# Kernel optimization log

Hardware: AMD Instinct MI355X
Metric: run time of the kernel (lower is better)

Reference implementation:

```python
import jax, jax.numpy as jnp
import numpy as np

N = 50000      # nodes
E = 800000     # edges per relation/layer
L = 2          # GCN layer_num
D = 128        # input_dim == output_dim


def setup_inputs() -> dict:
    key = jax.random.key(0)
    ks = jax.random.split(key, 11)
    x = jax.random.normal(ks[0], (N, D), jnp.float32)
    hidden = jax.random.normal(ks[1], (N, D), jnp.float32)
    adj_src = jax.random.randint(ks[2], (L, E), 0, N)
    adj_dst = jax.random.randint(ks[3], (L, E), 0, N)
    adj_w = jax.random.uniform(ks[4], (L, E), jnp.float32)
    std = 1.0 / np.sqrt(D)  # reset_parameters: uniform(-std, std)
    def u(k, shape):
        return jax.random.uniform(k, shape, jnp.float32, -std, std)
    gcn_W = u(ks[5], (L, D, D))
    gcn_b = u(ks[6], (L, D))
    x2h_W = u(ks[7], (D, 3 * D))
    x2h_b = u(ks[8], (3 * D,))
    h2h_W = u(ks[9], (D, 3 * D))
    h2h_b = u(ks[10], (3 * D,))
    return dict(x=x, hidden=hidden, adj_src=adj_src, adj_dst=adj_dst, adj_w=adj_w,
                gcn_W=gcn_W, gcn_b=gcn_b, x2h_W=x2h_W, x2h_b=x2h_b,
                h2h_W=h2h_W, h2h_b=h2h_b)


def reference(x, hidden, adj_src, adj_dst, adj_w, gcn_W, gcn_b,
              x2h_W, x2h_b, h2h_W, h2h_b):
    # MRGCN: layer_num GCN layers, layer l uses relation l's sparse adjacency.
    h = x
    for l in range(L):
        support = h @ gcn_W[l]                              # [N, D]
        msg = support[adj_src[l]] * adj_w[l][:, None]       # [E, D] irregular gather
        agg = jax.ops.segment_sum(msg, adj_dst[l], num_segments=N)  # spmm scatter-add
        h = jax.nn.relu(agg + gcn_b[l])
    # GRU gate chain (dropout=0 / eval mode)
    gate_x = h @ x2h_W + x2h_b                              # [N, 3D]
    gate_h = hidden @ h2h_W + h2h_b                         # [N, 3D]
    i_r, i_i, i_n = jnp.split(gate_x, 3, axis=1)
    h_r, h_i, h_n = jnp.split(gate_h, 3, axis=1)
    resetgate = jax.nn.sigmoid(i_r + h_r)
    inputgate = jax.nn.sigmoid(i_i + h_i)
    newgate = jnp.tanh(i_n + resetgate * h_n)
    hy = newgate + inputgate * (hidden - newgate)
    return hy
```

## Files before the change

### kernel.cpp

```cpp
#include <hip/hip_runtime.h>

#define D 128
#define RPW 8
#define ROWS_PB 32

typedef __attribute__((ext_vector_type(8))) short short8;
typedef __attribute__((ext_vector_type(4))) float f32x4;

static __device__ __forceinline__ ushort f2bf(float f) {
    unsigned u = __float_as_uint(f);
    unsigned r = (u + 0x7fffu + ((u >> 16) & 1u)) >> 16;
    return (ushort)r;
}

static __device__ __forceinline__ void gemm_body(float* sw, float (*sh)[D],
                                                 const float* __restrict__ in,
                                                 const float* __restrict__ W,
                                                 ushort* __restrict__ outb,
                                                 int N, int bid, int tid) {
    int row0 = bid * ROWS_PB;
    for (int j = tid; j < D * D / 4; j += 256)
        ((float4*)sw)[j] = ((const float4*)W)[j];
    for (int i = tid; i < ROWS_PB * (D / 4); i += 256) {
        int r = i >> 5, c4 = i & 31;
        int row = row0 + r;
        float4 v = (row < N) ? ((const float4*)(in + (size_t)row * D))[c4]
                             : make_float4(0.f, 0.f, 0.f, 0.f);
        ((float4*)sh)[i] = v;
    }
    __syncthreads();
    int wid = tid >> 6, lane = tid & 63;
    int rb = wid * RPW;
    float acc0[RPW], acc1[RPW];
#pragma unroll
    for (int r = 0; r < RPW; ++r) { acc0[r] = 0.f; acc1[r] = 0.f; }
    for (int k = 0; k < D; k += 4) {
        float w0[4], w1[4];
#pragma unroll
        for (int kk = 0; kk < 4; ++kk) {
            w0[kk] = sw[(k + kk) * D + lane];
            w1[kk] = sw[(k + kk) * D + lane + 64];
        }
#pragma unroll
        for (int r = 0; r < RPW; ++r) {
            float4 a4 = *(const float4*)&sh[rb + r][k];
            acc0[r] = fmaf(a4.x, w0[0], acc0[r]); acc1[r] = fmaf(a4.x, w1[0], acc1[r]);
            acc0[r] = fmaf(a4.y, w0[1], acc0[r]); acc1[r] = fmaf(a4.y, w1[1], acc1[r]);
            acc0[r] = fmaf(a4.z, w0[2], acc0[r]); acc1[r] = fmaf(a4.z, w1[2], acc1[r]);
            acc0[r] = fmaf(a4.w, w0[3], acc0[r]); acc1[r] = fmaf(a4.w, w1[3], acc1[r]);
        }
    }
#pragma unroll
    for (int r = 0; r < RPW; ++r) {
        int row = row0 + rb + r;
        if (row < N) {
            outb[(size_t)row * D + lane] = f2bf(acc0[r]);
            outb[(size_t)row * D + lane + 64] = f2bf(acc1[r]);
        }
    }
}

__global__ __launch_bounds__(256) void fused_sgc(const float* __restrict__ x,
                                                 const float* __restrict__ W0,
                                                 ushort* __restrict__ Abf, int N,
                                                 const int* __restrict__ adj_dst,
                                                 int* __restrict__ counts,
                                                 ushort* __restrict__ pl, int E2,
                                                 int E, int GB,
                                                 const float* __restrict__ Wx,
                                                 const float* __restrict__ Wh,
                                                 ushort* __restrict__ wxt,
                                                 ushort* __restrict__ wht) {
    __shared__ float sw[D * D];
    __shared__ float sh[ROWS_PB][D];
    int bid = blockIdx.x, tid = threadIdx.x;
    int five = GB * 5;
    if (bid < five) {
        int g = bid / 5, j = bid - g * 5;
        if (j == 0) {
            gemm_body(sw, sh, x, W0, Abf, N, g, tid);
        } else {
            int i = (g * 4 + j - 1) * 256 + tid;
            if (i < E2) {
                int off = (i >= E) ? N : 0;
                pl[i] = (ushort)atomicAdd(&counts[off + adj_dst[i]], 1);
            }
        }
    } else {
        int i = (bid - five) * 256 + tid;
        if (i < 384 * 128) {
            int c = i >> 7, k = i & 127;
            wxt[i] = f2bf(Wx[(size_t)k * 384 + c]);
            wht[i] = f2bf(Wh[(size_t)k * 384 + c]);
        }
    }
}

__global__ void zero_int4(int4* __restrict__ p, int n4) {
    int i = blockIdx.x * blockDim.x + threadIdx.x;
    if (i < n4) p[i] = make_int4(0, 0, 0, 0);
}

__global__ __launch_bounds__(256) void scan_partial(const int4* __restrict__ counts4,
                                                    int* __restrict__ bsum) {
    int b = blockIdx.x, t = threadIdx.x;
    int4 c0 = counts4[(size_t)b * 512 + t * 2];
    int4 c1 = counts4[(size_t)b * 512 + t * 2 + 1];
    int s = c0.x + c0.y + c0.z + c0.w + c1.x + c1.y + c1.z + c1.w;
#pragma unroll
    for (int d = 1; d < 64; d <<= 1) s += __shfl_xor(s, d);
    __shared__ int ws[4];
    if ((t & 63) == 0) ws[t >> 6] = s;
    __syncthreads();
    if (t == 0) bsum[b] = ws[0] + ws[1] + ws[2] + ws[3];
}

__global__ void scan_base(const int* __restrict__ bsum, int* __restrict__ bbase, int nb) {
    int lane = threadIdx.x;
    int run = 0;
    for (int c = 0; c < nb; c += 64) {
        int v = (c + lane < nb) ? bsum[c + lane] : 0;
        int inc = v;
#pragma unroll
        for (int d = 1; d < 64; d <<= 1) {
            int y = __shfl_up(inc, d);
            if (lane >= d) inc += y;
        }
        if (c + lane < nb) bbase[c + lane] = run + inc - v;
        run += __shfl(inc, 63);
    }
}

__global__ __launch_bounds__(256) void scan_apply(const int4* __restrict__ counts4,
                                                  const int* __restrict__ bbase,
                                                  int4* __restrict__ off4) {
    __shared__ int ts[256];
    int b = blockIdx.x, t = threadIdx.x;
    int4 c0 = counts4[(size_t)b * 512 + t * 2];
    int4 c1 = counts4[(size_t)b * 512 + t * 2 + 1];
    int s = c0.x + c0.y + c0.z + c0.w + c1.x + c1.y + c1.z + c1.w;
    ts[t] = s;
    __syncthreads();
    for (int d = 1; d < 256; d <<= 1) {
        int x = ts[t];
        int y = (t >= d) ? ts[t - d] : 0;
        __syncthreads();
        ts[t] = x + y;
        __syncthreads();
    }
    int base = bbase[b] + ((t == 0) ? 0 : ts[t - 1]);
    int4 o0, o1;
    o0.x = base;
    o0.y = o0.x + c0.x;
    o0.z = o0.y + c0.y;
    o0.w = o0.z + c0.z;
    o1.x = o0.w + c0.w;
    o1.y = o1.x + c1.x;
    o1.z = o1.y + c1.y;
    o1.w = o1.z + c1.z;
    off4[(size_t)b * 512 + t * 2] = o0;
    off4[(size_t)b * 512 + t * 2 + 1] = o1;
}

__global__ void place2_kernel(const int* __restrict__ src, const int* __restrict__ dst,
                              const float* __restrict__ w,
                              const int* __restrict__ offsets2,
                              const ushort* __restrict__ pl,
                              int2* __restrict__ srcw0, int2* __restrict__ srcw1,
                              int E, int E2, int N) {
    int i = blockIdx.x * blockDim.x + threadIdx.x;
    if (i >= E2) return;
    int l1 = i >= E;
    int node = dst[i];
    int p = offsets2[(l1 ? N : 0) + node] - (l1 ? E : 0) + (int)pl[i];
    int2 v = make_int2(src[i], __float_as_int(w[i]));
    (l1 ? srcw1 : srcw0)[p] = v;
}

static __device__ __forceinline__ void gather_row(const ushort* __restrict__ base,
                                                  const int2* __restrict__ srcw,
                                                  int lo, int hi,
                                                  float& ax, float& ay) {
    ax = 0.f; ay = 0.f;
    int j = lo;
    for (; j + 8 <= hi; j += 8) {
        int2 s[8];
        uint v[8];
#pragma unroll
        for (int u = 0; u < 8; ++u) s[u] = srcw[j + u];
#pragma unroll
        for (int u = 0; u < 8; ++u)
            v[u] = *(const uint*)(base + ((size_t)s[u].x << 7));
#pragma unroll
        for (int u = 0; u < 8; ++u) {
            float wt = __int_as_float(s[u].y);
            ax = fmaf(wt, __uint_as_float(v[u] << 16), ax);
            ay = fmaf(wt, __uint_as_float(v[u] & 0xffff0000u), ay);
        }
    }
    for (; j < hi; ++j) {
        int2 sw = srcw[j];
        float wt = __int_as_float(sw.y);
        uint v = *(const uint*)(base + ((size_t)sw.x << 7));
        ax = fmaf(wt, __uint_as_float(v << 16), ax);
        ay = fmaf(wt, __uint_as_float(v & 0xffff0000u), ay);
    }
}

__global__ __launch_bounds__(256) void gather_gemm(const ushort* __restrict__ supb,
                                                   const int2* __restrict__ srcw,
                                                   const int* __restrict__ offsets,
                                                   const float* __restrict__ bias,
                                                   const float* __restrict__ W1,
                                                   ushort* __restrict__ outb, int N) {
    __shared__ float sw1[D * D];
    __shared__ float rowbuf[4][D];
    int tid = threadIdx.x;
    for (int j = tid; j < D * D / 4; j += 256)
        ((float4*)sw1)[j] = ((const float4*)W1)[j];
    __syncthreads();
    int wid = tid >> 6, lane = tid & 63;
    int c = lane * 2;
    const ushort* base = supb + c;
#pragma unroll
    for (int r = 0; r < 4; ++r) {
        int node = blockIdx.x * 16 + wid * 4 + r;
        if (node >= N) break;
        int lo = offsets[node], hi = offsets[node + 1];
        float ax, ay;
        gather_row(base, srcw, lo, hi, ax, ay);
        float2 bi = *(const float2*)(bias + c);
        rowbuf[wid][c] = fmaxf(ax + bi.x, 0.f);
        rowbuf[wid][c + 1] = fmaxf(ay + bi.y, 0.f);
        float acc0 = 0.f, acc1 = 0.f;
        for (int k = 0; k < D; k += 4) {
            float4 rv = *(const float4*)&rowbuf[wid][k];
            acc0 = fmaf(rv.x, sw1[(k + 0) * D + lane], acc0);
            acc1 = fmaf(rv.x, sw1[(k + 0) * D + lane + 64], acc1);
            acc0 = fmaf(rv.y, sw1[(k + 1) * D + lane], acc0);
            acc1 = fmaf(rv.y, sw1[(k + 1) * D + lane + 64], acc1);
            acc0 = fmaf(rv.z, sw1[(k + 2) * D + lane], acc0);
            acc1 = fmaf(rv.z, sw1[(k + 2) * D + lane + 64], acc1);
            acc0 = fmaf(rv.w, sw1[(k + 3) * D + lane], acc0);
            acc1 = fmaf(rv.w, sw1[(k + 3) * D + lane + 64], acc1);
        }
        outb[(size_t)node * D + lane] = f2bf(acc0);
        outb[(size_t)node * D + lane + 64] = f2bf(acc1);
    }
}

__global__ void gather_nodes_bf(const ushort* __restrict__ supb,
                                const int2* __restrict__ srcw,
                                const int* __restrict__ offsets, int sub,
                                const float* __restrict__ bias,
                                ushort* __restrict__ outb, int N) {
    int node = (blockIdx.x * blockDim.x + threadIdx.x) >> 6;
    int lane = threadIdx.x & 63;
    if (node >= N) return;
    int lo = offsets[node] - sub, hi = offsets[node + 1] - sub;
    int c = lane * 2;
    float ax, ay;
    gather_row(supb + c, srcw, lo, hi, ax, ay);
    float2 bi = *(const float2*)(bias + c);
    uint pk = ((uint)f2bf(fmaxf(ay + bi.y, 0.f)) << 16) | (uint)f2bf(fmaxf(ax + bi.x, 0.f));
    *(uint*)(outb + (size_t)node * D + c) = pk;
}

#define QROWS 192
#define KPAD 136
__global__ __launch_bounds__(256) void gru_mfma_lds(const ushort* __restrict__ hb,
                                                    const float* __restrict__ hidden,
                                                    const ushort* __restrict__ wxt,
                                                    const ushort* __restrict__ wht,
                                                    const float* __restrict__ bx,
                                                    const float* __restrict__ bh,
                                                    float* __restrict__ out, int N) {
    __shared__ ushort lw[QROWS * KPAD];
    int tid = threadIdx.x;
    int wid = tid >> 6, lane = tid & 63;
    int nstripes = (N + 15) >> 4;
    int stripe = blockIdx.x * 4 + wid;
    bool live = stripe < nstripes;
    int row0 = stripe * 16;
    int lr = lane & 15;
    int lk = (lane >> 4) * 8;

    short8 Ah[4], Ad[4];
    if (live) {
        const ushort* hrow = hb + (size_t)(row0 + lr) * D + lk;
        const float* drow = hidden + (size_t)(row0 + lr) * D + lk;
#pragma unroll
        for (int ks = 0; ks < 4; ++ks) {
            Ah[ks] = *(const short8*)(hrow + ks * 32);
            float4 c0 = *(const float4*)(drow + ks * 32);
            float4 c1 = *(const float4*)(drow + ks * 32 + 4);
            short8 vc;
            vc[0] = f2bf(c0.x); vc[1] = f2bf(c0.y); vc[2] = f2bf(c0.z); vc[3] = f2bf(c0.w);
            vc[4] = f2bf(c1.x); vc[5] = f2bf(c1.y); vc[6] = f2bf(c1.z); vc[7] = f2bf(c1.w);
            Ad[ks] = vc;
        }
    }
    int orow = row0 + (lane >> 4) * 4;

    for (int q = 0; q < 4; ++q) {
        if (q) __syncthreads();
        for (int j = tid; j < QROWS * 16; j += 256) {
            int chunk = j & 15;
            int row = j >> 4;
            int mat = row >= 96;
            int r = row - (mat ? 96 : 0);
            int g = r >> 5;
            int c = r & 31;
            const ushort* srcp = (mat ? wht : wxt)
                               + ((size_t)(g * 128 + q * 32 + c) << 7) + (chunk << 3);
            *(short8*)&lw[row * KPAD + chunk * 8] = *(const short8*)srcp;
        }
        __syncthreads();
        if (!live) continue;

#pragma unroll
        for (int mt = 0; mt < 2; ++mt) {
            int cl = mt * 16 + lr;
            const ushort* bx0 = lw + (0 * 32 + cl) * KPAD + lk;
            const ushort* bx1 = lw + (1 * 32 + cl) * KPAD + lk;
            const ushort* bx2 = lw + (2 * 32 + cl) * KPAD + lk;
            const ushort* bh0 = lw + ((96 + 0 * 32) + cl) * KPAD + lk;
            const ushort* bh1 = lw + ((96 + 1 * 32) + cl) * KPAD + lk;
            const ushort* bh2 = lw + ((96 + 2 * 32) + cl) * KPAD + lk;
            f32x4 ax0{}, ax1{}, ax2{}, ah0{}, ah1{}, ah2{};
#pragma unroll
            for (int ks = 0; ks < 4; ++ks) {
                short8 w0 = *(const short8*)(bx0 + ks * 32);
                short8 w1 = *(const short8*)(bx1 + ks * 32);
                short8 w2 = *(const short8*)(bx2 + ks * 32);
                short8 v0 = *(const short8*)(bh0 + ks * 32);
                short8 v1 = *(const short8*)(bh1 + ks * 32);
                short8 v2 = *(const short8*)(bh2 + ks * 32);
                ax0 = __builtin_amdgcn_mfma_f32_16x16x32_bf16(Ah[ks], w0, ax0, 0, 0, 0);
                ax1 = __builtin_amdgcn_mfma_f32_16x16x32_bf16(Ah[ks], w1, ax1, 0, 0, 0);
                ax2 = __builtin_amdgcn_mfma_f32_16x16x32_bf16(Ah[ks], w2, ax2, 0, 0, 0);
                ah0 = __builtin_amdgcn_mfma_f32_16x16x32_bf16(Ad[ks], v0, ah0, 0, 0, 0);
                ah1 = __builtin_amdgcn_mfma_f32_16x16x32_bf16(Ad[ks], v1, ah1, 0, 0, 0);
                ah2 = __builtin_amdgcn_mfma_f32_16x16x32_bf16(Ad[ks], v2, ah2, 0, 0, 0);
            }
            int col = q * 32 + mt * 16 + lr;
            float bxr = bx[col], bxi = bx[col + 128], bxn = bx[col + 256];
            float bhr = bh[col], bhi = bh[col + 128], bhn = bh[col + 256];
#pragma unroll
            for (int r = 0; r < 4; ++r) {
                int row = orow + r;
                if (row < N) {
                    float ir = ax0[r] + bxr, hr = ah0[r] + bhr;
                    float ii = ax1[r] + bxi, hi = ah1[r] + bhi;
                    float in_ = ax2[r] + bxn, hn = ah2[r] + bhn;
                    float rg = 1.f / (1.f + __expf(-(ir + hr)));
                    float ig = 1.f / (1.f + __expf(-(ii + hi)));
                    float nx = in_ + rg * hn;
                    float ng = 1.f - 2.f / (__expf(2.f * nx) + 1.f);
                    float hv = hidden[(size_t)row * D + col];
                    out[(size_t)row * D + col] = ng + ig * (hv - ng);
                }
            }
        }
    }
}

extern "C" void kernel_launch(void* const* d_in, const int* in_sizes, int n_in,
                              void* d_out, int out_size, void* d_ws, size_t ws_size,
                              hipStream_t stream) {
    const float* x      = (const float*)d_in[0];
    const float* hidden = (const float*)d_in[1];
    const int*   adj_src = (const int*)d_in[2];
    const int*   adj_dst = (const int*)d_in[3];
    const float* adj_w   = (const float*)d_in[4];
    const float* gcn_W   = (const float*)d_in[5];
    const float* gcn_b   = (const float*)d_in[6];
    const float* x2h_W   = (const float*)d_in[7];
    const float* x2h_b   = (const float*)d_in[8];
    const float* h2h_W   = (const float*)d_in[9];
    const float* h2h_b   = (const float*)d_in[10];
    float* out = (float*)d_out;

    const int L = 2;
    const int N = in_sizes[0] / D;
    const int E = in_sizes[2] / L;
    const size_t nd = (size_t)N * D;

    const int twoN   = 2 * N;
    const int NB     = (twoN + 2047) / 2048;
    const int padded = NB * 2048;

    char* ws = (char*)d_ws;
    ushort* Abf     = (ushort*)ws;                ws += nd * 2;
    ushort* Abf2    = (ushort*)ws;                ws += nd * 2;
    ushort* Bbf     = (ushort*)ws;                ws += nd * 2;
    int*   counts2  = (int*)ws;                   ws += (size_t)padded * 4;
    int*   offsets2 = (int*)ws;                   ws += ((size_t)padded + 64) * 4;
    int*   bsum     = (int*)ws;                   ws += ((size_t)NB + 64) * 4;
    int*   bbase    = (int*)ws;                   ws += ((size_t)NB + 64) * 4;
    int2*  srcw0    = (int2*)ws;                  ws += (size_t)E * 8;
    int2*  srcw1    = (int2*)ws;                  ws += (size_t)E * 8;
    ushort* pl      = (ushort*)ws;                ws += (size_t)2 * E * 2;
    ushort* wxt     = (ushort*)ws;                ws += (size_t)384 * 128 * 2;
    ushort* wht     = (ushort*)ws;                ws += (size_t)384 * 128 * 2;

    dim3 blk(256);
    int batch_blocks = (N + ROWS_PB - 1) / ROWS_PB;
    int gat_blocks   = (N + 3) / 4;
    int e2_blocks    = (2 * E + 255) / 256;
    int zero_blocks  = (padded / 4 + 255) / 256;
    int convw_blocks = (384 * 128 + 255) / 256;
    int gg_blocks    = (N + 15) / 16;
    int nstripes     = (N + 15) / 16;
    int gru_blocks   = (nstripes + 3) / 4;

    zero_int4<<<zero_blocks, blk, 0, stream>>>((int4*)counts2, padded / 4);
    fused_sgc<<<batch_blocks * 5 + convw_blocks, blk, 0, stream>>>(
        x, gcn_W, Abf, N, adj_dst, counts2, pl, 2 * E, E, batch_blocks,
        x2h_W, h2h_W, wxt, wht);
    scan_partial<<<NB, blk, 0, stream>>>((const int4*)counts2, bsum);
    scan_base<<<1, 64, 0, stream>>>(bsum, bbase, NB);
    scan_apply<<<NB, blk, 0, stream>>>((const int4*)counts2, bbase, (int4*)offsets2);
    place2_kernel<<<e2_blocks, blk, 0, stream>>>(adj_src, adj_dst, adj_w, offsets2, pl,
                                                 srcw0, srcw1, E, 2 * E, N);
    gather_gemm<<<gg_blocks, blk, 0, stream>>>(Abf, srcw0, offsets2, gcn_b,
                                               gcn_W + (size_t)D * D, Abf2, N);
    gather_nodes_bf<<<gat_blocks, blk, 0, stream>>>(Abf2, srcw1, offsets2 + N, E,
                                                    gcn_b + D, Bbf, N);
    gru_mfma_lds<<<gru_blocks, blk, 0, stream>>>(Bbf, hidden, wxt, wht, x2h_b, h2h_b,
                                                 out, N);
}
```

Baseline: 373.4 us.

## Split fused gather+GEMM into separate gather and row-batched GEMM kernels

```diff
diff --git a/kernel.cpp b/kernel.cpp
--- a/kernel.cpp
+++ b/kernel.cpp
@@ -11,6 +11,40 @@
     unsigned u = __float_as_uint(f);
     unsigned r = (u + 0x7fffu + ((u >> 16) & 1u)) >> 16;
     return (ushort)r;
+}
+
+static __device__ __forceinline__ void gemm_compute(const float* sw, float (*sh)[D],
+                                                    ushort* __restrict__ outb,
+                                                    int N, int row0, int tid) {
+    int wid = tid >> 6, lane = tid & 63;
+    int rb = wid * RPW;
+    float acc0[RPW], acc1[RPW];
+#pragma unroll
+    for (int r = 0; r < RPW; ++r) { acc0[r] = 0.f; acc1[r] = 0.f; }
+    for (int k = 0; k < D; k += 4) {
+        float w0[4], w1[4];
+#pragma unroll
+        for (int kk = 0; kk < 4; ++kk) {
+            w0[kk] = sw[(k + kk) * D + lane];
+            w1[kk] = sw[(k + kk) * D + lane + 64];
+        }
+#pragma unroll
+        for (int r = 0; r < RPW; ++r) {
+            float4 a4 = *(const float4*)&sh[rb + r][k];
+            acc0[r] = fmaf(a4.x, w0[0], acc0[r]); acc1[r] = fmaf(a4.x, w1[0], acc1[r]);
+            acc0[r] = fmaf(a4.y, w0[1], acc0[r]); acc1[r] = fmaf(a4.y, w1[1], acc1[r]);
+            acc0[r] = fmaf(a4.z, w0[2], acc0[r]); acc1[r] = fmaf(a4.z, w1[2], acc1[r]);
+            acc0[r] = fmaf(a4.w, w0[3], acc0[r]); acc1[r] = fmaf(a4.w, w1[3], acc1[r]);
+        }
+    }
+#pragma unroll
+    for (int r = 0; r < RPW; ++r) {
+        int row = row0 + rb + r;
+        if (row < N) {
+            outb[(size_t)row * D + lane] = f2bf(acc0[r]);
+            outb[(size_t)row * D + lane + 64] = f2bf(acc1[r]);
+        }
+    }
 }
 
 static __device__ __forceinline__ void gemm_body(float* sw, float (*sh)[D],
@@ -29,35 +63,7 @@
         ((float4*)sh)[i] = v;
     }
     __syncthreads();
-    int wid = tid >> 6, lane = tid & 63;
-    int rb = wid * RPW;
-    float acc0[RPW], acc1[RPW];
-#pragma unroll
-    for (int r = 0; r < RPW; ++r) { acc0[r] = 0.f; acc1[r] = 0.f; }
-    for (int k = 0; k < D; k += 4) {
-        float w0[4], w1[4];
-#pragma unroll
-        for (int kk = 0; kk < 4; ++kk) {
-            w0[kk] = sw[(k + kk) * D + lane];
-            w1[kk] = sw[(k + kk) * D + lane + 64];
-        }
-#pragma unroll
-        for (int r = 0; r < RPW; ++r) {
-            float4 a4 = *(const float4*)&sh[rb + r][k];
-            acc0[r] = fmaf(a4.x, w0[0], acc0[r]); acc1[r] = fmaf(a4.x, w1[0], acc1[r]);
-            acc0[r] = fmaf(a4.y, w0[1], acc0[r]); acc1[r] = fmaf(a4.y, w1[1], acc1[r]);
-            acc0[r] = fmaf(a4.z, w0[2], acc0[r]); acc1[r] = fmaf(a4.z, w1[2], acc1[r]);
-            acc0[r] = fmaf(a4.w, w0[3], acc0[r]); acc1[r] = fmaf(a4.w, w1[3], acc1[r]);
-        }
-    }
-#pragma unroll
-    for (int r = 0; r < RPW; ++r) {
-        int row = row0 + rb + r;
-        if (row < N) {
-            outb[(size_t)row * D + lane] = f2bf(acc0[r]);
-            outb[(size_t)row * D + lane + 64] = f2bf(acc1[r]);
-        }
-    }
+    gemm_compute(sw, sh, outb, N, row0, tid);
 }
 
 __global__ __launch_bounds__(256) void fused_sgc(const float* __restrict__ x,
@@ -96,6 +102,34 @@
     }
 }
 
+__global__ __launch_bounds__(256) void gemm_rowbatch_bfin(const ushort* __restrict__ in,
+                                                          const float* __restrict__ W,
+                                                          ushort* __restrict__ outb, int N) {
+    __shared__ float sw[D * D];
+    __shared__ float sh[ROWS_PB][D];
+    int tid = threadIdx.x;
+    int row0 = blockIdx.x * ROWS_PB;
+    for (int j = tid; j < D * D / 4; j += 256)
+        ((float4*)sw)[j] = ((const float4*)W)[j];
+    for (int i = tid; i < ROWS_PB * (D / 4); i += 256) {
+        int r = i >> 5, c4 = i & 31;
+        int row = row0 + r;
+        float4 v;
+        if (row < N) {
+            uint2 u = ((const uint2*)(in + (size_t)row * D))[c4];
+            v.x = __uint_as_float(u.x << 16);
+            v.y = __uint_as_float(u.x & 0xffff0000u);
+            v.z = __uint_as_float(u.y << 16);
+            v.w = __uint_as_float(u.y & 0xffff0000u);
+        } else {
+            v = make_float4(0.f, 0.f, 0.f, 0.f);
+        }
+        ((float4*)sh)[i] = v;
+    }
+    __syncthreads();
+    gemm_compute(sw, sh, outb, N, row0, tid);
+}
+
 __global__ void zero_int4(int4* __restrict__ p, int n4) {
     int i = blockIdx.x * blockDim.x + threadIdx.x;
     if (i < n4) p[i] = make_int4(0, 0, 0, 0);
@@ -204,48 +238,6 @@
         uint v = *(const uint*)(base + ((size_t)sw.x << 7));
         ax = fmaf(wt, __uint_as_float(v << 16), ax);
         ay = fmaf(wt, __uint_as_float(v & 0xffff0000u), ay);
-    }
-}
-
-__global__ __launch_bounds__(256) void gather_gemm(const ushort* __restrict__ supb,
-                                                   const int2* __restrict__ srcw,
-                                                   const int* __restrict__ offsets,
-                                                   const float* __restrict__ bias,
-                                                   const float* __restrict__ W1,
-                                                   ushort* __restrict__ outb, int N) {
-    __shared__ float sw1[D * D];
-    __shared__ float rowbuf[4][D];
-    int tid = threadIdx.x;
-    for (int j = tid; j < D * D / 4; j += 256)
-        ((float4*)sw1)[j] = ((const float4*)W1)[j];
-    __syncthreads();
-    int wid = tid >> 6, lane = tid & 63;
-    int c = lane * 2;
-    const ushort* base = supb + c;
-#pragma unroll
-    for (int r = 0; r < 4; ++r) {
-        int node = blockIdx.x * 16 + wid * 4 + r;
-        if (node >= N) break;
-        int lo = offsets[node], hi = offsets[node + 1];
-        float ax, ay;
-        gather_row(base, srcw, lo, hi, ax, ay);
-        float2 bi = *(const float2*)(bias + c);
-        rowbuf[wid][c] = fmaxf(ax + bi.x, 0.f);
-        rowbuf[wid][c + 1] = fmaxf(ay + bi.y, 0.f);
-        float acc0 = 0.f, acc1 = 0.f;
-        for (int k = 0; k < D; k += 4) {
-            float4 rv = *(const float4*)&rowbuf[wid][k];
-            acc0 = fmaf(rv.x, sw1[(k + 0) * D + lane], acc0);
-            acc1 = fmaf(rv.x, sw1[(k + 0) * D + lane + 64], acc1);
-            acc0 = fmaf(rv.y, sw1[(k + 1) * D + lane], acc0);
-            acc1 = fmaf(rv.y, sw1[(k + 1) * D + lane + 64], acc1);
-            acc0 = fmaf(rv.z, sw1[(k + 2) * D + lane], acc0);
-            acc1 = fmaf(rv.z, sw1[(k + 2) * D + lane + 64], acc1);
-            acc0 = fmaf(rv.w, sw1[(k + 3) * D + lane], acc0);
-            acc1 = fmaf(rv.w, sw1[(k + 3) * D + lane + 64], acc1);
-        }
-        outb[(size_t)node * D + lane] = f2bf(acc0);
-        outb[(size_t)node * D + lane + 64] = f2bf(acc1);
     }
 }
 
@@ -391,9 +383,8 @@
     const int padded = NB * 2048;
 
     char* ws = (char*)d_ws;
-    ushort* Abf     = (ushort*)ws;                ws += nd * 2;
-    ushort* Abf2    = (ushort*)ws;                ws += nd * 2;
-    ushort* Bbf     = (ushort*)ws;                ws += nd * 2;
+    ushort* P       = (ushort*)ws;                ws += nd * 2;
+    ushort* Q       = (ushort*)ws;                ws += nd * 2;
     int*   counts2  = (int*)ws;                   ws += (size_t)padded * 4;
     int*   offsets2 = (int*)ws;                   ws += ((size_t)padded + 64) * 4;
     int*   bsum     = (int*)ws;                   ws += ((size_t)NB + 64) * 4;
@@ -410,23 +401,24 @@
     int e2_blocks    = (2 * E + 255) / 256;
     int zero_blocks  = (padded / 4 + 255) / 256;
     int convw_blocks = (384 * 128 + 255) / 256;
-    int gg_blocks    = (N + 15) / 16;
     int nstripes     = (N + 15) / 16;
     int gru_blocks   = (nstripes + 3) / 4;
 
     zero_int4<<<zero_blocks, blk, 0, stream>>>((int4*)counts2, padded / 4);
     fused_sgc<<<batch_blocks * 5 + convw_blocks, blk, 0, stream>>>(
-        x, gcn_W, Abf, N, adj_dst, counts2, pl, 2 * E, E, batch_blocks,
+        x, gcn_W, P, N, adj_dst, counts2, pl, 2 * E, E, batch_blocks,
         x2h_W, h2h_W, wxt, wht);
     scan_partial<<<NB, blk, 0, stream>>>((const int4*)counts2, bsum);
     scan_base<<<1, 64, 0, stream>>>(bsum, bbase, NB);
     scan_apply<<<NB, blk, 0, stream>>>((const int4*)counts2, bbase, (int4*)offsets2);
     place2_kernel<<<e2_blocks, blk, 0, stream>>>(adj_src, adj_dst, adj_w, offsets2, pl,
                                                  srcw0, srcw1, E, 2 * E, N);
-    gather_gemm<<<gg_blocks, blk, 0, stream>>>(Abf, srcw0, offsets2, gcn_b,
-                                               gcn_W + (size_t)D * D, Abf2, N);
-    gather_nodes_bf<<<gat_blocks, blk, 0, stream>>>(Abf2, srcw1, offsets2 + N, E,
-                                                    gcn_b + D, Bbf, N);
-    gru_mfma_lds<<<gru_blocks, blk, 0, stream>>>(Bbf, hidden, wxt, wht, x2h_b, h2h_b,
+    gather_nodes_bf<<<gat_blocks, blk, 0, stream>>>(P, srcw0, offsets2, 0,
+                                                    gcn_b, Q, N);
+    gemm_rowbatch_bfin<<<batch_blocks, blk, 0, stream>>>(Q, gcn_W + (size_t)D * D,
+                                                         P, N);
+    gather_nodes_bf<<<gat_blocks, blk, 0, stream>>>(P, srcw1, offsets2 + N, E,
+                                                    gcn_b + D, Q, N);
+    gru_mfma_lds<<<gru_blocks, blk, 0, stream>>>(Q, hidden, wxt, wht, x2h_b, h2h_b,
                                                  out, N);
 }
```

Measured after the change: 306.9 us. 17.8% less time.
